# Kernel optimization log

Measured on AMD Instinct MI355X. Metric: run time of the kernel, lower is better.

## Reference

```python
import jax, jax.numpy as jnp
import numpy as np

D = 100  # input_size


def _gru_scan(x, h0, wi, wh, bi, bh):
    # x: [B,T,Din], h0: [B,H], wi: [3H,Din], wh: [3H,H]  (PyTorch r,z,n gate order)
    xw = jnp.einsum('btd,gd->btg', x, wi) + bi  # [B,T,3H]
    def step(h, xt):
        gh = h @ wh.T + bh
        xr, xz, xn = jnp.split(xt, 3, axis=-1)
        hr, hz, hn = jnp.split(gh, 3, axis=-1)
        r = jax.nn.sigmoid(xr + hr)
        z = jax.nn.sigmoid(xz + hz)
        n = jnp.tanh(xn + r * hn)
        hn2 = (1 - z) * n + z * h
        return hn2, hn2
    _, ys = jax.lax.scan(step, h0, jnp.swapaxes(xw, 0, 1))
    return jnp.swapaxes(ys, 0, 1)  # [B,T,H]


def _bigru(x, wi, wh, bi, bh):
    B = x.shape[0]
    H = wh.shape[-1]
    h0 = jnp.zeros((B, H), x.dtype)
    f = _gru_scan(x, h0, wi[0], wh[0], bi[0], bh[0])
    b = _gru_scan(x[:, ::-1], h0, wi[1], wh[1], bi[1], bh[1])[:, ::-1]
    return jnp.concatenate([f, b], axis=-1)


def _gru_cell(x, h, wi, wh, bi, bh):
    gx = x @ wi.T + bi
    gh = h @ wh.T + bh
    xr, xz, xn = jnp.split(gx, 3, axis=-1)
    hr, hz, hn = jnp.split(gh, 3, axis=-1)
    r = jax.nn.sigmoid(xr + hr)
    z = jax.nn.sigmoid(xz + hz)
    n = jnp.tanh(xn + r * hn)
    return (1 - z) * n + z * h


def setup_inputs() -> dict:
    key = jax.random.key(0)
    ks = iter(jax.random.split(key, 40))
    def n(shape, s=0.08):
        return (jax.random.normal(next(ks), shape) * s).astype(jnp.float32)
    B, T, L, V = 32, 512, 64, 400000
    inp = {
        'x_word': jax.random.randint(next(ks), (B, T), 0, V),
        'x_query': jax.random.randint(next(ks), (B, L), 0, V),
        'embed': n((V, D), 0.3),
        'ctx_wi': n((2, 3 * D, D)), 'ctx_wh': n((2, 3 * D, D)),
        'ctx_bi': n((2, 3 * D)), 'ctx_bh': n((2, 3 * D)),
        'mod0_wi': n((2, 3 * D, 8 * D)), 'mod0_wh': n((2, 3 * D, D)),
        'mod0_bi': n((2, 3 * D)), 'mod0_bh': n((2, 3 * D)),
        'mod1_wi': n((2, 3 * D, 2 * D)), 'mod1_wh': n((2, 3 * D, D)),
        'mod1_bi': n((2, 3 * D)), 'mod1_bh': n((2, 3 * D)),
        'w_sim': n((6 * D,)),
        'enc_wi': n((12 * D, 2 * D)), 'enc_wh': n((12 * D, 4 * D)),
        'enc_bi': n((12 * D,)), 'enc_bh': n((12 * D,)),
        'dec_wi': n((12 * D, 2 * D)), 'dec_wh': n((12 * D, 4 * D)),
        'dec_bi': n((12 * D,)), 'dec_bh': n((12 * D,)),
        'w1': n((2 * D, 4 * D)), 'w2': n((2 * D, 4 * D)), 'vt': n((2 * D,)),
    }
    return inp


def reference(x_word, x_query, embed, ctx_wi, ctx_wh, ctx_bi, ctx_bh,
              mod0_wi, mod0_wh, mod0_bi, mod0_bh, mod1_wi, mod1_wh, mod1_bi, mod1_bh,
              w_sim, enc_wi, enc_wh, enc_bi, enc_bh, dec_wi, dec_wh, dec_bi, dec_bh,
              w1, w2, vt):
    B, T = x_word.shape
    # shared bidirectional context encoder over both context and query
    h = _bigru(embed[x_word], ctx_wi, ctx_wh, ctx_bi, ctx_bh)   # [B,T,2D]
    u = _bigru(embed[x_query], ctx_wi, ctx_wh, ctx_bi, ctx_bh)  # [B,L,2D]
    # trilinear similarity W @ cat(h,u,h*u), fused (no [B,T,L,6D] materialization)
    w1s, w2s, w3s = jnp.split(w_sim, 3)
    S = (jnp.einsum('btd,d->bt', h, w1s)[:, :, None]
         + jnp.einsum('bld,d->bl', u, w2s)[:, None, :]
         + jnp.einsum('btd,bld->btl', h * w3s, u))               # [B,T,L]
    c2q = jnp.einsum('btl,bld->btd', jax.nn.softmax(S, axis=-1), u)
    b_att = jax.nn.softmax(jnp.max(S, axis=2), axis=-1)          # [B,T]
    q2c = jnp.einsum('bt,btd->bd', b_att, h)[:, None, :]         # [B,1,2D]
    G = jnp.concatenate([h, c2q, h * c2q, h * q2c], axis=-1)     # [B,T,8D]
    # 2-layer bidirectional modeling GRU
    M = _bigru(G, mod0_wi, mod0_wh, mod0_bi, mod0_bh)
    M = _bigru(M, mod1_wi, mod1_wh, mod1_bi, mod1_bh)            # [B,T,2D]
    # pointer network
    enc = _gru_scan(M, jnp.zeros((B, 4 * D), M.dtype), enc_wi, enc_wh, enc_bi, enc_bh)  # [B,T,4D]
    enc_w1 = jnp.einsum('bth,ph->btp', enc, w1)                  # precompute W1 @ enc
    hid = jnp.zeros((B, 4 * D), M.dtype)
    dec_in = jnp.zeros((B, 2 * D), M.dtype)  # never updated (as in original)
    probs = []
    for _ in range(2):  # answers = 2 (start, end)
        hid = _gru_cell(dec_in, hid, dec_wi, dec_wh, dec_bi, dec_bh)
        blend = jnp.tanh(enc_w1 + (hid @ w2.T)[:, None, :])      # [B,T,2D]
        out = jnp.einsum('btp,p->bt', blend, vt)
        probs.append(jax.nn.log_softmax(out, axis=-1))
    return jnp.stack(probs, axis=1)  # [B,2,T]
```

## Files before the change

### kernel.cpp

```cpp
#include <hip/hip_runtime.h>
#include <hip/hip_bf16.h>

typedef __hip_bfloat16 bf16;
typedef unsigned long long u64;
typedef __attribute__((ext_vector_type(8))) short s8v;
typedef __attribute__((ext_vector_type(4))) short s4v;
typedef __attribute__((ext_vector_type(4))) float f4v;

#define DEV __device__ __forceinline__

DEV float to_f32(float x) { return x; }
DEV float to_f32(bf16 x) { return __bfloat162float(x); }
DEV void store_c(float* p, float v) { *p = v; }
DEV void store_c(bf16* p, float v) { *p = __float2bfloat16(v); }
DEV float sigmf(float x) { return 1.f / (1.f + __expf(-x)); }
DEV short f2bs(float x) { bf16 h = __float2bfloat16(x); return *(short*)&h; }

__global__ void cvt_all(const float* __restrict__ s0, bf16* __restrict__ d0,
                        const float* __restrict__ s1, bf16* __restrict__ d1,
                        const float* __restrict__ s2, bf16* __restrict__ d2,
                        const float* __restrict__ s3, bf16* __restrict__ d3,
                        const float* __restrict__ s4, bf16* __restrict__ d4) {
  int i = blockIdx.x * blockDim.x + threadIdx.x;
  if (i < 60000) d0[i] = __float2bfloat16(s0[i]);
  i -= 60000;
  if (i >= 0 && i < 480000) d1[i] = __float2bfloat16(s1[i]);
  i -= 480000;
  if (i >= 0 && i < 120000) d2[i] = __float2bfloat16(s2[i]);
  i -= 120000;
  if (i >= 0 && i < 240000) d3[i] = __float2bfloat16(s3[i]);
  i -= 240000;
  if (i >= 0 && i < 80000) d4[i] = __float2bfloat16(s4[i]);
}

template <typename TC, bool HAS_BIAS, bool GATHER>
__global__ __launch_bounds__(256) void gemm_mfma(
    const bf16* __restrict__ A, const int* __restrict__ idx,
    const float* __restrict__ embedp, const bf16* __restrict__ W,
    const float* __restrict__ bias, TC* __restrict__ C,
    int M, int N, int K) {
  __shared__ short Als[2][128 * 32];
  __shared__ short Wls[2][128 * 32];
  const int tid = threadIdx.x;
  const int m0 = blockIdx.x * 128;
  const int n0 = blockIdx.y * 128;
  const int lane = tid & 63;
  const int wv = tid >> 6;
  const int wm = wv >> 1, wn = wv & 1;
  const int lq = lane >> 4, lr = lane & 15;
  const int row2 = tid >> 1;
  const int half = tid & 1;

  int vrow = 0;
  if (GATHER) vrow = idx[m0 + row2];
  const int nrow = n0 + row2;

  s4v ra[4], rw[4];
  auto load_regs = [&](int k0) {
#pragma unroll
    for (int ss = 0; ss < 4; ++ss) {
      int kk = k0 + half * 16 + ss * 4;
      if (GATHER) {
        if (kk + 4 <= K) {
          float4 a4 = *(const float4*)(embedp + (size_t)vrow * 100 + kk);
          ra[ss] = (s4v){f2bs(a4.x), f2bs(a4.y), f2bs(a4.z), f2bs(a4.w)};
        } else {
          s4v v = {0, 0, 0, 0};
#pragma unroll
          for (int j = 0; j < 4; ++j)
            if (kk + j < K) v[j] = f2bs(embedp[(size_t)vrow * 100 + kk + j]);
          ra[ss] = v;
        }
      } else {
        const short* src = (const short*)(A + (size_t)(m0 + row2) * K + kk);
        if (kk + 4 <= K) {
          ra[ss] = *(const s4v*)src;
        } else {
          s4v v = {0, 0, 0, 0};
#pragma unroll
          for (int j = 0; j < 4; ++j)
            if (kk + j < K) v[j] = src[j];
          ra[ss] = v;
        }
      }
      if (nrow < N) {
        const short* src = (const short*)(W + (size_t)nrow * K + kk);
        if (kk + 4 <= K) {
          rw[ss] = *(const s4v*)src;
        } else {
          s4v v = {0, 0, 0, 0};
#pragma unroll
          for (int j = 0; j < 4; ++j)
            if (kk + j < K) v[j] = src[j];
          rw[ss] = v;
        }
      } else {
        rw[ss] = (s4v){0, 0, 0, 0};
      }
    }
  };
  auto write_lds = [&](int buf) {
#pragma unroll
    for (int ss = 0; ss < 4; ++ss) {
      *(s4v*)&Als[buf][row2 * 32 + half * 16 + ss * 4] = ra[ss];
      *(s4v*)&Wls[buf][row2 * 32 + half * 16 + ss * 4] = rw[ss];
    }
  };

  f4v acc[4][4];
#pragma unroll
  for (int i = 0; i < 4; ++i)
#pragma unroll
    for (int j = 0; j < 4; ++j) acc[i][j] = (f4v){0.f, 0.f, 0.f, 0.f};

  const int nk = (K + 31) / 32;
  load_regs(0);
  write_lds(0);
  __syncthreads();
  int cur = 0;
  for (int ki = 0; ki < nk; ++ki) {
    if (ki + 1 < nk) load_regs((ki + 1) * 32);
    s8v af[4], bfr[4];
#pragma unroll
    for (int mi = 0; mi < 4; ++mi) {
      int r = wm * 64 + mi * 16 + lr;
      af[mi] = *(const s8v*)&Als[cur][r * 32 + lq * 8];
    }
#pragma unroll
    for (int ni = 0; ni < 4; ++ni) {
      int r = wn * 64 + ni * 16 + lr;
      bfr[ni] = *(const s8v*)&Wls[cur][r * 32 + lq * 8];
    }
#pragma unroll
    for (int mi = 0; mi < 4; ++mi)
#pragma unroll
      for (int ni = 0; ni < 4; ++ni)
        acc[mi][ni] = __builtin_amdgcn_mfma_f32_16x16x32_bf16(af[mi], bfr[ni], acc[mi][ni], 0, 0, 0);
    if (ki + 1 < nk) write_lds(cur ^ 1);
    __syncthreads();
    cur ^= 1;
  }
#pragma unroll
  for (int mi = 0; mi < 4; ++mi) {
#pragma unroll
    for (int ni = 0; ni < 4; ++ni) {
      int n = n0 + wn * 64 + ni * 16 + lr;
      if (n >= N) continue;
      float bv = HAS_BIAS ? bias[n] : 0.f;
#pragma unroll
      for (int r = 0; r < 4; ++r) {
        int m = m0 + wm * 64 + mi * 16 + lq * 4 + r;
        store_c(&C[(size_t)m * N + n], acc[mi][ni][r] + bv);
      }
    }
  }
}

template <typename TO>
__global__ __launch_bounds__(192) void gru_scan100_dual(
    const bf16* __restrict__ xw0, const bf16* __restrict__ xw1,
    const float* __restrict__ wh,
    const float* __restrict__ bh,
    TO* __restrict__ out0, TO* __restrict__ out1,
    int T0, int T1) {
  const int b = blockIdx.x;
  const int y = blockIdx.y;
  const int which = y >> 1, dir = y & 1;
  const bf16* xw = which ? xw1 : xw0;
  TO* out = which ? out1 : out0;
  const int T = which ? T1 : T0;
  __shared__ float h_s[100];
  __shared__ float g_s[300];
  const int tid = threadIdx.x;
  float w0[100], w1[100];
  float bias0 = 0.f, bias1 = 0.f;
  if (tid < 150) {
    const float* wr0 = wh + (size_t)dir * 30000 + (size_t)(2 * tid) * 100;
#pragma unroll
    for (int c = 0; c < 25; ++c) {
      float4 v = *(const float4*)(wr0 + 4 * c);
      w0[4 * c] = v.x; w0[4 * c + 1] = v.y; w0[4 * c + 2] = v.z; w0[4 * c + 3] = v.w;
      float4 u = *(const float4*)(wr0 + 100 + 4 * c);
      w1[4 * c] = u.x; w1[4 * c + 1] = u.y; w1[4 * c + 2] = u.z; w1[4 * c + 3] = u.w;
    }
    bias0 = bh[dir * 300 + 2 * tid];
    bias1 = bh[dir * 300 + 2 * tid + 1];
  }
  if (tid < 100) h_s[tid] = 0.f;
  float pxr = 0.f, pxz = 0.f, pxn = 0.f;
  if (tid < 100) {
    int t0 = dir ? (T - 1) : 0;
    size_t base = ((size_t)b * T + t0) * 600 + dir * 300;
    pxr = to_f32(xw[base + tid]);
    pxz = to_f32(xw[base + 100 + tid]);
    pxn = to_f32(xw[base + 200 + tid]);
  }
  __syncthreads();
  for (int step = 0; step < T; ++step) {
    int t = dir ? (T - 1 - step) : step;
    if (tid < 150) {
      float a0 = bias0, a1 = 0.f, a2 = 0.f, a3 = 0.f;
      float b0 = bias1, b1 = 0.f, b2 = 0.f, b3 = 0.f;
#pragma unroll
      for (int c = 0; c < 25; ++c) {
        float4 h4 = *(const float4*)(&h_s[4 * c]);
        a0 += w0[4 * c] * h4.x; a1 += w0[4 * c + 1] * h4.y;
        a2 += w0[4 * c + 2] * h4.z; a3 += w0[4 * c + 3] * h4.w;
        b0 += w1[4 * c] * h4.x; b1 += w1[4 * c + 1] * h4.y;
        b2 += w1[4 * c + 2] * h4.z; b3 += w1[4 * c + 3] * h4.w;
      }
      g_s[2 * tid] = (a0 + a1) + (a2 + a3);
      g_s[2 * tid + 1] = (b0 + b1) + (b2 + b3);
    }
    __syncthreads();
    if (tid < 100) {
      float rr = sigmf(pxr + g_s[tid]);
      float zz = sigmf(pxz + g_s[100 + tid]);
      float nn = tanhf(pxn + rr * g_s[200 + tid]);
      float hn = (1.f - zz) * nn + zz * h_s[tid];
      h_s[tid] = hn;
      store_c(&out[((size_t)b * T + t) * 200 + dir * 100 + tid], hn);
      if (step + 1 < T) {
        int tn = dir ? (T - 2 - step) : (step + 1);
        size_t basen = ((size_t)b * T + tn) * 600 + dir * 300;
        pxr = to_f32(xw[basen + tid]);
        pxz = to_f32(xw[basen + 100 + tid]);
        pxn = to_f32(xw[basen + 200 + tid]);
      }
    }
    __syncthreads();
  }
}

__global__ __launch_bounds__(640) void gru_scan_enc_tag(
    const bf16* __restrict__ xw,
    const float* __restrict__ wh,
    const float* __restrict__ bh,
    bf16* __restrict__ out,
    u64* __restrict__ hx,
    int T) {
  const int b = blockIdx.x, s = blockIdx.y;
  __shared__ float h_s[400];
  __shared__ float g_s[150];
  const int tid = threadIdx.x;
  const int g = tid >> 2, p = tid & 3;
  const bool active = (tid < 600);
  float w[100];
  float bias = 0.f;
  if (active) {
    int i = g % 50, grp = g / 50;
    int gidx = grp * 400 + s * 50 + i;
    const float* wrow = wh + (size_t)gidx * 400 + p * 100;
#pragma unroll
    for (int c = 0; c < 25; ++c) {
      float4 v = *(const float4*)(wrow + 4 * c);
      w[4 * c] = v.x; w[4 * c + 1] = v.y; w[4 * c + 2] = v.z; w[4 * c + 3] = v.w;
    }
    if (p == 0) bias = bh[gidx];
  }
  for (int k = tid; k < 400; k += 640) h_s[k] = 0.f;
  const int myi = s * 50 + tid;
  float pxr = 0.f, pxz = 0.f, pxn = 0.f;
  if (tid < 50) {
    size_t base0 = (size_t)b * T * 1200;
    pxr = to_f32(xw[base0 + myi]);
    pxz = to_f32(xw[base0 + 400 + myi]);
    pxn = to_f32(xw[base0 + 800 + myi]);
  }
  __syncthreads();

  for (int t = 0; t < T; ++t) {
    if (active) {
      const int hb = p * 100;
      float4 hbuf[25];
#pragma unroll
      for (int c = 0; c < 25; ++c) hbuf[c] = *(const float4*)(&h_s[hb + 4 * c]);
      float a0 = bias, a1 = 0.f, a2 = 0.f, a3 = 0.f;
#pragma unroll
      for (int c = 0; c < 25; ++c) {
        a0 += w[4 * c] * hbuf[c].x; a1 += w[4 * c + 1] * hbuf[c].y;
        a2 += w[4 * c + 2] * hbuf[c].z; a3 += w[4 * c + 3] * hbuf[c].w;
      }
      float acc = (a0 + a1) + (a2 + a3);
      acc += __shfl_xor(acc, 1);
      acc += __shfl_xor(acc, 2);
      if (p == 0) g_s[g] = acc;
    }
    __syncthreads();
    const int par = (t + 1) & 1;
    u64* hxp = hx + ((size_t)b * 2 + par) * 400;
    if (tid < 50) {
      float rr = sigmf(pxr + g_s[tid]);
      float zz = sigmf(pxz + g_s[50 + tid]);
      float nn = tanhf(pxn + rr * g_s[100 + tid]);
      float hn = (1.f - zz) * nn + zz * h_s[myi];
      out[((size_t)b * T + t) * 400 + myi] = __float2bfloat16(hn);
      h_s[myi] = hn;
      u64 pack = (u64)__float_as_uint(hn) | ((u64)(unsigned)(t + 1) << 32);
      __hip_atomic_store(&hxp[myi], pack, __ATOMIC_RELAXED, __HIP_MEMORY_SCOPE_AGENT);
      if (t + 1 < T) {
        size_t basen = ((size_t)b * T + (t + 1)) * 1200;
        pxr = to_f32(xw[basen + myi]);
        pxz = to_f32(xw[basen + 400 + myi]);
        pxn = to_f32(xw[basen + 800 + myi]);
      }
    }
    if (tid < 400 && (tid / 50) != s) {
      const u64* src = &hxp[tid];
      u64 v;
      for (;;) {
        v = __hip_atomic_load(src, __ATOMIC_RELAXED, __HIP_MEMORY_SCOPE_AGENT);
        if ((unsigned)(v >> 32) == (unsigned)(t + 1)) break;
        __builtin_amdgcn_s_sleep(1);
      }
      h_s[tid] = __uint_as_float((unsigned)v);
    }
    __syncthreads();
  }
}

__global__ __launch_bounds__(256) void attn_main(
    const float* __restrict__ h, const float* __restrict__ u,
    const float* __restrict__ w_sim, float* __restrict__ c2q,
    float* __restrict__ smax, int T) {
  const int b = blockIdx.x;
  const int t0 = blockIdx.y * 32;
  __shared__ float u_s[64 * 201];
  __shared__ float w1_s[200], w2_s[200], w3_s[200];
  __shared__ float th_s[32], tu_s[64];
  __shared__ float hw3_s[200];
  __shared__ float Sp[4][64];
  __shared__ float A_s[64];
  const int tid = threadIdx.x;
  for (int i = tid; i < 64 * 200; i += 256) {
    int l = i / 200, d = i - l * 200;
    u_s[l * 201 + d] = u[((size_t)b * 64 + l) * 200 + d];
  }
  if (tid < 200) {
    w1_s[tid] = w_sim[tid];
    w2_s[tid] = w_sim[200 + tid];
    w3_s[tid] = w_sim[400 + tid];
  }
  __syncthreads();
  {
    int r = tid >> 2, sg = tid & 3;
    float p = 0.f;
    for (int j = 0; j < 50; ++j) p += u_s[r * 201 + sg * 50 + j] * w2_s[sg * 50 + j];
    p += __shfl_down(p, 2);
    p += __shfl_down(p, 1);
    if (sg == 0) tu_s[r] = p;
  }
  {
    int r = tid >> 3, sg = tid & 7;
    float p = 0.f;
    const float* hr = h + ((size_t)b * T + t0 + r) * 200 + sg * 25;
    for (int j = 0; j < 25; ++j) p += hr[j] * w1_s[sg * 25 + j];
    p += __shfl_down(p, 4);
    p += __shfl_down(p, 2);
    p += __shfl_down(p, 1);
    if (sg == 0) th_s[r] = p;
  }
  __syncthreads();
  for (int tt = 0; tt < 32; ++tt) {
    int t = t0 + tt;
    if (tid < 200) hw3_s[tid] = h[((size_t)b * T + t) * 200 + tid] * w3_s[tid];
    __syncthreads();
    int l = tid & 63, q = tid >> 6;
    float p = 0.f;
    for (int d = q * 50; d < q * 50 + 50; ++d) p += hw3_s[d] * u_s[l * 201 + d];
    Sp[q][l] = p;
    __syncthreads();
    if (tid < 64) {
      float s = th_s[tt] + tu_s[l] + Sp[0][l] + Sp[1][l] + Sp[2][l] + Sp[3][l];
      float m = s;
      for (int off = 32; off; off >>= 1) m = fmaxf(m, __shfl_xor(m, off));
      float e = __expf(s - m);
      float ssum = e;
      for (int off = 32; off; off >>= 1) ssum += __shfl_xor(ssum, off);
      A_s[l] = e / ssum;
      if (l == 0) smax[b * T + t] = m;
    }
    __syncthreads();
    if (tid < 200) {
      float acc = 0.f;
      for (int l2 = 0; l2 < 64; ++l2) acc += A_s[l2] * u_s[l2 * 201 + tid];
      c2q[((size_t)b * T + t) * 200 + tid] = acc;
    }
    __syncthreads();
  }
}

__global__ __launch_bounds__(256) void softmax_q2c(
    const float* __restrict__ smaxv, const float* __restrict__ h,
    float* __restrict__ q2c, int T) {
  int b = blockIdx.x;
  int tid = threadIdx.x;
  __shared__ float red[256];
  __shared__ float batt_s[512];
  float m = -1e30f;
  for (int t = tid; t < T; t += 256) m = fmaxf(m, smaxv[b * T + t]);
  red[tid] = m;
  __syncthreads();
  for (int s = 128; s; s >>= 1) {
    if (tid < s) red[tid] = fmaxf(red[tid], red[tid + s]);
    __syncthreads();
  }
  m = red[0];
  __syncthreads();
  float sum = 0.f;
  for (int t = tid; t < T; t += 256) {
    float e = __expf(smaxv[b * T + t] - m);
    batt_s[t] = e;
    sum += e;
  }
  red[tid] = sum;
  __syncthreads();
  for (int s = 128; s; s >>= 1) {
    if (tid < s) red[tid] += red[tid + s];
    __syncthreads();
  }
  float inv = 1.f / red[0];
  __syncthreads();
  if (tid < 200) {
    float acc = 0.f;
    for (int t = 0; t < T; ++t) acc += batt_s[t] * h[((size_t)b * T + t) * 200 + tid];
    q2c[b * 200 + tid] = acc * inv;
  }
}

__global__ void build_G(const float* __restrict__ h, const float* __restrict__ c2q,
                        const float* __restrict__ q2c, bf16* __restrict__ G, int T) {
  size_t i = (size_t)blockIdx.x * blockDim.x + threadIdx.x;
  if (i >= (size_t)32 * T * 200) return;
  size_t row = i / 200;
  int d = (int)(i - row * 200);
  int b = (int)(row / T);
  float hv = h[i];
  float cv = c2q[i];
  float qv = q2c[b * 200 + d];
  bf16* g = G + row * 800;
  g[d] = __float2bfloat16(hv);
  g[200 + d] = __float2bfloat16(cv);
  g[400 + d] = __float2bfloat16(hv * cv);
  g[600 + d] = __float2bfloat16(hv * qv);
}

__global__ __launch_bounds__(512) void decoder_small(
    const float* __restrict__ dwh, const float* __restrict__ dbi,
    const float* __restrict__ dbh, const float* __restrict__ w2,
    float* __restrict__ d2out) {
  __shared__ float hid[400];
  __shared__ float hid2[400];
  __shared__ float gh[1200];
  const int tid = threadIdx.x;
  if (tid < 400) {
    float r = sigmf(dbi[tid] + dbh[tid]);
    float z = sigmf(dbi[400 + tid] + dbh[400 + tid]);
    float n = tanhf(dbi[800 + tid] + r * dbh[800 + tid]);
    hid[tid] = (1.f - z) * n;
  }
  __syncthreads();
  if (tid < 200) {
    float a = 0.f;
    for (int k = 0; k < 400; ++k) a += w2[(size_t)tid * 400 + k] * hid[k];
    d2out[tid] = a;
  }
  for (int j = tid; j < 1200; j += 512) {
    float a = dbh[j];
    for (int k = 0; k < 400; ++k) a += dwh[(size_t)j * 400 + k] * hid[k];
    gh[j] = a;
  }
  __syncthreads();
  if (tid < 400) {
    float r = sigmf(dbi[tid] + gh[tid]);
    float z = sigmf(dbi[400 + tid] + gh[400 + tid]);
    float n = tanhf(dbi[800 + tid] + r * gh[800 + tid]);
    hid2[tid] = (1.f - z) * n + z * hid[tid];
  }
  __syncthreads();
  if (tid < 200) {
    float a = 0.f;
    for (int k = 0; k < 400; ++k) a += w2[(size_t)tid * 400 + k] * hid2[k];
    d2out[200 + tid] = a;
  }
}

__global__ __launch_bounds__(512) void logits_lsm(
    const float* __restrict__ encw1, const float* __restrict__ d2,
    const float* __restrict__ vt, float* __restrict__ outp, int T) {
  int b = blockIdx.x;
  __shared__ float lg[2][512];
  __shared__ float red[512];
  const int tid = threadIdx.x;
  const int wave = tid >> 6, lane = tid & 63;
  for (int r = wave; r < T; r += 8) {
    const float* e = encw1 + ((size_t)b * T + r) * 200;
    float s0 = 0.f, s1 = 0.f;
    for (int p = lane; p < 200; p += 64) {
      float ev = e[p], v = vt[p];
      s0 += tanhf(ev + d2[p]) * v;
      s1 += tanhf(ev + d2[200 + p]) * v;
    }
    for (int off = 32; off; off >>= 1) {
      s0 += __shfl_down(s0, off);
      s1 += __shfl_down(s1, off);
    }
    if (lane == 0) { lg[0][r] = s0; lg[1][r] = s1; }
  }
  __syncthreads();
  for (int it = 0; it < 2; ++it) {
    red[tid] = lg[it][tid];
    __syncthreads();
    for (int s = 256; s; s >>= 1) {
      if (tid < s) red[tid] = fmaxf(red[tid], red[tid + s]);
      __syncthreads();
    }
    float m = red[0];
    __syncthreads();
    red[tid] = __expf(lg[it][tid] - m);
    __syncthreads();
    for (int s = 256; s; s >>= 1) {
      if (tid < s) red[tid] += red[tid + s];
      __syncthreads();
    }
    float lse = m + __logf(red[0]);
    __syncthreads();
    outp[((size_t)b * 2 + it) * T + tid] = lg[it][tid] - lse;
  }
}

extern "C" void kernel_launch(void* const* d_in, const int* in_sizes, int n_in,
                              void* d_out, int out_size, void* d_ws, size_t ws_size,
                              hipStream_t stream) {
  (void)in_sizes; (void)n_in; (void)out_size; (void)ws_size;
  const int B = 32, T = 512, L = 64;
  const int BT = B * T;
  const int BL = B * L;

  const int* x_word = (const int*)d_in[0];
  const int* x_query = (const int*)d_in[1];
  const float* embed = (const float*)d_in[2];
  const float* ctx_wi = (const float*)d_in[3];
  const float* ctx_wh = (const float*)d_in[4];
  const float* ctx_bi = (const float*)d_in[5];
  const float* ctx_bh = (const float*)d_in[6];
  const float* mod0_wi = (const float*)d_in[7];
  const float* mod0_wh = (const float*)d_in[8];
  const float* mod0_bi = (const float*)d_in[9];
  const float* mod0_bh = (const float*)d_in[10];
  const float* mod1_wi = (const float*)d_in[11];
  const float* mod1_wh = (const float*)d_in[12];
  const float* mod1_bi = (const float*)d_in[13];
  const float* mod1_bh = (const float*)d_in[14];
  const float* w_sim = (const float*)d_in[15];
  const float* enc_wi = (const float*)d_in[16];
  const float* enc_wh = (const float*)d_in[17];
  const float* enc_bi = (const float*)d_in[18];
  const float* enc_bh = (const float*)d_in[19];
  const float* dec_wh = (const float*)d_in[21];
  const float* dec_bi = (const float*)d_in[22];
  const float* dec_bh = (const float*)d_in[23];
  const float* w1 = (const float*)d_in[24];
  const float* w2 = (const float*)d_in[25];
  const float* vt = (const float*)d_in[26];
  float* out_f = (float*)d_out;

  char* ws = (char*)d_ws;
  size_t off = 0;
  auto alloc = [&](size_t bytes) -> void* {
    void* p = ws + off;
    off += (bytes + 255) & ~(size_t)255;
    return p;
  };
  u64* hx = (u64*)alloc((size_t)B * 2 * 400 * 8);
  bf16* ctx_wibf = (bf16*)alloc((size_t)60000 * 2);
  bf16* mod0_wibf = (bf16*)alloc((size_t)480000 * 2);
  bf16* mod1_wibf = (bf16*)alloc((size_t)120000 * 2);
  bf16* enc_wibf = (bf16*)alloc((size_t)240000 * 2);
  bf16* w1bf = (bf16*)alloc((size_t)80000 * 2);
  char* RA = (char*)alloc((size_t)BT * 1200 * 2);
  bf16* xwFB = (bf16*)RA;
  bf16* xwe = (bf16*)RA;
  bf16* xwq = (bf16*)alloc((size_t)BL * 600 * 2);
  char* RB = (char*)alloc((size_t)BT * 800 * 2);
  bf16* G = (bf16*)RB;
  bf16* enc_outbf = (bf16*)RB;
  char* RC = (char*)alloc((size_t)2 * BT * 200 * 4);
  float* h_cat = (float*)RC;
  float* c2q = (float*)(RC + (size_t)BT * 200 * 4);
  bf16* M0bf = (bf16*)c2q;
  bf16* Mxbf = (bf16*)h_cat;
  float* encw1 = c2q;
  float* u_cat = (float*)alloc((size_t)BL * 200 * 4);
  float* smaxb = (float*)alloc((size_t)BT * 4);
  float* q2cb = (float*)alloc((size_t)B * 200 * 4);
  float* d2 = (float*)alloc((size_t)400 * 4);

  hipMemsetAsync(hx, 0, (size_t)B * 2 * 400 * 8, stream);

  cvt_all<<<(980000 + 255) / 256, 256, 0, stream>>>(ctx_wi, ctx_wibf, mod0_wi, mod0_wibf,
                                                    mod1_wi, mod1_wibf, enc_wi, enc_wibf,
                                                    w1, w1bf);

  gemm_mfma<bf16, true, true><<<dim3(BT / 128, 5), 256, 0, stream>>>(
      nullptr, x_word, embed, ctx_wibf, ctx_bi, xwFB, BT, 600, 100);
  gemm_mfma<bf16, true, true><<<dim3(BL / 128, 5), 256, 0, stream>>>(
      nullptr, x_query, embed, ctx_wibf, ctx_bi, xwq, BL, 600, 100);

  gru_scan100_dual<float><<<dim3(B, 4), 192, 0, stream>>>(
      xwFB, xwq, ctx_wh, ctx_bh, h_cat, u_cat, T, L);

  attn_main<<<dim3(B, T / 32), 256, 0, stream>>>(h_cat, u_cat, w_sim, c2q, smaxb, T);
  softmax_q2c<<<B, 256, 0, stream>>>(smaxb, h_cat, q2cb, T);
  build_G<<<(BT * 200 + 255) / 256, 256, 0, stream>>>(h_cat, c2q, q2cb, G, T);

  gemm_mfma<bf16, true, false><<<dim3(BT / 128, 5), 256, 0, stream>>>(
      G, nullptr, nullptr, mod0_wibf, mod0_bi, xwFB, BT, 600, 800);
  gru_scan100_dual<bf16><<<dim3(B, 2), 192, 0, stream>>>(
      xwFB, nullptr, mod0_wh, mod0_bh, M0bf, nullptr, T, T);

  gemm_mfma<bf16, true, false><<<dim3(BT / 128, 5), 256, 0, stream>>>(
      M0bf, nullptr, nullptr, mod1_wibf, mod1_bi, xwFB, BT, 600, 200);
  gru_scan100_dual<bf16><<<dim3(B, 2), 192, 0, stream>>>(
      xwFB, nullptr, mod1_wh, mod1_bh, Mxbf, nullptr, T, T);

  gemm_mfma<bf16, true, false><<<dim3(BT / 128, 10), 256, 0, stream>>>(
      Mxbf, nullptr, nullptr, enc_wibf, enc_bi, xwe, BT, 1200, 200);
  gru_scan_enc_tag<<<dim3(B, 8), 640, 0, stream>>>(xwe, enc_wh, enc_bh, enc_outbf, hx, T);
  gemm_mfma<float, false, false><<<dim3(BT / 128, 2), 256, 0, stream>>>(
      enc_outbf, nullptr, nullptr, w1bf, nullptr, encw1, BT, 200, 400);

  decoder_small<<<1, 512, 0, stream>>>(dec_wh, dec_bi, dec_bh, w2, d2);
  logits_lsm<<<B, 512, 0, stream>>>(encw1, d2, vt, out_f, T);
}
```

Before: 3.185 ms.

## Restructure GRU-100 scan to one barrier per step with split-K shuffle reduce

Reorganizes the 100-wide GRU scan so each pair of threads owns one hidden unit's r, z and n gate rows, each lane holding half of the K dimension. The two halves are combined with a lane shuffle, and the hidden state is double-buffered in shared memory. This removes the shared gate buffer and one of the two block barriers per timestep on this latency-bound sequential loop. In exchange it uses 200 active threads instead of 150, and the gate nonlinearity still runs on only half the lanes.

```diff
diff --git a/kernel.cpp b/kernel.cpp
--- a/kernel.cpp
+++ b/kernel.cpp
@@ -157,7 +157,7 @@
 }
 
 template <typename TO>
-__global__ __launch_bounds__(192) void gru_scan100_dual(
+__global__ __launch_bounds__(256) void gru_scan100_1b(
     const bf16* __restrict__ xw0, const bf16* __restrict__ xw1,
     const float* __restrict__ wh,
     const float* __restrict__ bh,
@@ -169,66 +169,78 @@
   const bf16* xw = which ? xw1 : xw0;
   TO* out = which ? out1 : out0;
   const int T = which ? T1 : T0;
-  __shared__ float h_s[100];
-  __shared__ float g_s[300];
+  __shared__ float h_s[2][100];
   const int tid = threadIdx.x;
-  float w0[100], w1[100];
-  float bias0 = 0.f, bias1 = 0.f;
-  if (tid < 150) {
-    const float* wr0 = wh + (size_t)dir * 30000 + (size_t)(2 * tid) * 100;
+  const int i = tid >> 1, half = tid & 1;
+  const bool act = (tid < 200);
+  float wr[50], wz[50], wn[50];
+  float br = 0.f, bz = 0.f, bn = 0.f;
+  if (act) {
+    const float* wb = wh + (size_t)dir * 30000;
+    const float* rowr = wb + (size_t)i * 100 + half * 50;
+    const float* rowz = wb + (size_t)(100 + i) * 100 + half * 50;
+    const float* rown = wb + (size_t)(200 + i) * 100 + half * 50;
 #pragma unroll
     for (int c = 0; c < 25; ++c) {
-      float4 v = *(const float4*)(wr0 + 4 * c);
-      w0[4 * c] = v.x; w0[4 * c + 1] = v.y; w0[4 * c + 2] = v.z; w0[4 * c + 3] = v.w;
-      float4 u = *(const float4*)(wr0 + 100 + 4 * c);
-      w1[4 * c] = u.x; w1[4 * c + 1] = u.y; w1[4 * c + 2] = u.z; w1[4 * c + 3] = u.w;
-    }
-    bias0 = bh[dir * 300 + 2 * tid];
-    bias1 = bh[dir * 300 + 2 * tid + 1];
-  }
-  if (tid < 100) h_s[tid] = 0.f;
+      float2 vr = *(const float2*)(rowr + 2 * c);
+      wr[2 * c] = vr.x; wr[2 * c + 1] = vr.y;
+      float2 vz = *(const float2*)(rowz + 2 * c);
+      wz[2 * c] = vz.x; wz[2 * c + 1] = vz.y;
+      float2 vn = *(const float2*)(rown + 2 * c);
+      wn[2 * c] = vn.x; wn[2 * c + 1] = vn.y;
+    }
+    if (half == 0) {
+      br = bh[dir * 300 + i];
+      bz = bh[dir * 300 + 100 + i];
+      bn = bh[dir * 300 + 200 + i];
+    }
+  }
+  if (tid < 100) h_s[0][tid] = 0.f;
   float pxr = 0.f, pxz = 0.f, pxn = 0.f;
-  if (tid < 100) {
+  if (act && half == 0) {
     int t0 = dir ? (T - 1) : 0;
     size_t base = ((size_t)b * T + t0) * 600 + dir * 300;
-    pxr = to_f32(xw[base + tid]);
-    pxz = to_f32(xw[base + 100 + tid]);
-    pxn = to_f32(xw[base + 200 + tid]);
-  }
-  __syncthreads();
+    pxr = to_f32(xw[base + i]);
+    pxz = to_f32(xw[base + 100 + i]);
+    pxn = to_f32(xw[base + 200 + i]);
+  }
+  __syncthreads();
+  int cur = 0;
   for (int step = 0; step < T; ++step) {
     int t = dir ? (T - 1 - step) : step;
-    if (tid < 150) {
-      float a0 = bias0, a1 = 0.f, a2 = 0.f, a3 = 0.f;
-      float b0 = bias1, b1 = 0.f, b2 = 0.f, b3 = 0.f;
+    if (act) {
+      const float* hp = &h_s[cur][half * 50];
+      float a0 = br, a1 = 0.f, z0 = bz, z1 = 0.f, n0 = bn, n1 = 0.f;
 #pragma unroll
       for (int c = 0; c < 25; ++c) {
-        float4 h4 = *(const float4*)(&h_s[4 * c]);
-        a0 += w0[4 * c] * h4.x; a1 += w0[4 * c + 1] * h4.y;
-        a2 += w0[4 * c + 2] * h4.z; a3 += w0[4 * c + 3] * h4.w;
-        b0 += w1[4 * c] * h4.x; b1 += w1[4 * c + 1] * h4.y;
-        b2 += w1[4 * c + 2] * h4.z; b3 += w1[4 * c + 3] * h4.w;
-      }
-      g_s[2 * tid] = (a0 + a1) + (a2 + a3);
-      g_s[2 * tid + 1] = (b0 + b1) + (b2 + b3);
-    }
-    __syncthreads();
-    if (tid < 100) {
-      float rr = sigmf(pxr + g_s[tid]);
-      float zz = sigmf(pxz + g_s[100 + tid]);
-      float nn = tanhf(pxn + rr * g_s[200 + tid]);
-      float hn = (1.f - zz) * nn + zz * h_s[tid];
-      h_s[tid] = hn;
-      store_c(&out[((size_t)b * T + t) * 200 + dir * 100 + tid], hn);
-      if (step + 1 < T) {
-        int tn = dir ? (T - 2 - step) : (step + 1);
-        size_t basen = ((size_t)b * T + tn) * 600 + dir * 300;
-        pxr = to_f32(xw[basen + tid]);
-        pxz = to_f32(xw[basen + 100 + tid]);
-        pxn = to_f32(xw[basen + 200 + tid]);
-      }
-    }
-    __syncthreads();
+        float2 h2 = *(const float2*)(hp + 2 * c);
+        a0 += wr[2 * c] * h2.x; a1 += wr[2 * c + 1] * h2.y;
+        z0 += wz[2 * c] * h2.x; z1 += wz[2 * c + 1] * h2.y;
+        n0 += wn[2 * c] * h2.x; n1 += wn[2 * c + 1] * h2.y;
+      }
+      float gr = a0 + a1, gz = z0 + z1, gn = n0 + n1;
+      gr += __shfl_xor(gr, 1);
+      gz += __shfl_xor(gz, 1);
+      gn += __shfl_xor(gn, 1);
+      if (half == 0) {
+        float hprev = h_s[cur][i];
+        float rr = sigmf(pxr + gr);
+        float zz = sigmf(pxz + gz);
+        float nn = tanhf(pxn + rr * gn);
+        float hn = (1.f - zz) * nn + zz * hprev;
+        h_s[cur ^ 1][i] = hn;
+        store_c(&out[((size_t)b * T + t) * 200 + dir * 100 + i], hn);
+        if (step + 1 < T) {
+          int tn = dir ? (T - 2 - step) : (step + 1);
+          size_t basen = ((size_t)b * T + tn) * 600 + dir * 300;
+          pxr = to_f32(xw[basen + i]);
+          pxz = to_f32(xw[basen + 100 + i]);
+          pxn = to_f32(xw[basen + 200 + i]);
+        }
+      }
+    }
+    __syncthreads();
+    cur ^= 1;
   }
 }
 
@@ -607,7 +619,7 @@
   gemm_mfma<bf16, true, true><<<dim3(BL / 128, 5), 256, 0, stream>>>(
       nullptr, x_query, embed, ctx_wibf, ctx_bi, xwq, BL, 600, 100);
 
-  gru_scan100_dual<float><<<dim3(B, 4), 192, 0, stream>>>(
+  gru_scan100_1b<float><<<dim3(B, 4), 256, 0, stream>>>(
       xwFB, xwq, ctx_wh, ctx_bh, h_cat, u_cat, T, L);
 
   attn_main<<<dim3(B, T / 32), 256, 0, stream>>>(h_cat, u_cat, w_sim, c2q, smaxb, T);
@@ -616,12 +628,12 @@
 
   gemm_mfma<bf16, true, false><<<dim3(BT / 128, 5), 256, 0, stream>>>(
       G, nullptr, nullptr, mod0_wibf, mod0_bi, xwFB, BT, 600, 800);
-  gru_scan100_dual<bf16><<<dim3(B, 2), 192, 0, stream>>>(
+  gru_scan100_1b<bf16><<<dim3(B, 2), 256, 0, stream>>>(
       xwFB, nullptr, mod0_wh, mod0_bh, M0bf, nullptr, T, T);
 
   gemm_mfma<bf16, true, false><<<dim3(BT / 128, 5), 256, 0, stream>>>(
       M0bf, nullptr, nullptr, mod1_wibf, mod1_bi, xwFB, BT, 600, 200);
-  gru_scan100_dual<bf16><<<dim3(B, 2), 192, 0, stream>>>(
+  gru_scan100_1b<bf16><<<dim3(B, 2), 256, 0, stream>>>(
       xwFB, nullptr, mod1_wh, mod1_bh, Mxbf, nullptr, T, T);
 
   gemm_mfma<bf16, true, false><<<dim3(BT / 128, 10), 256, 0, stream>>>(
```

Measured after the change: 2.897 ms. 9.0% less time.
